# Optimization experiments

Hardware: AMD Instinct MI355X
Metric: run time of the kernel (lower is better)

## Reference

```python
import jax, jax.numpy as jnp
import numpy as np

N_NODES = 100000  # static segment count for segment_sum
DEGREE = 2        # polynomial degree of the Laplacian filter


def setup_inputs() -> dict:
    key = jax.random.key(0)
    k1, k2, k3, k4 = jax.random.split(key, 4)
    N, E, C = N_NODES, 1600000, 32
    x = jax.random.normal(k1, (N, C), dtype=jnp.float32)
    weights = jax.random.normal(k2, (1 + DEGREE,), dtype=jnp.float32)
    edge_src = jax.random.randint(k3, (E,), 0, N, dtype=jnp.int32)
    edge_dst = jax.random.randint(k4, (E,), 0, N, dtype=jnp.int32)
    return {"x": x, "weights": weights, "edge_src": edge_src, "edge_dst": edge_dst}


def reference(x, weights, edge_src, edge_dst):
    """y = (w0 * I + w1 * L + ... + w_d * L^d) @ x with L = D - A,
    computed by the recurrence t_k = L @ t_{k-1} (never materializing L^k)."""
    N = N_NODES
    # node degrees: D[i] = number of edges landing on i
    deg = jax.ops.segment_sum(jnp.ones_like(edge_src, dtype=x.dtype), edge_dst,
                              num_segments=N)  # [N]

    def lap_matvec(t):
        # (L @ t)[i] = deg[i] * t[i] - sum_{(s->i) in E} t[s]
        agg = jax.ops.segment_sum(t[edge_src], edge_dst, num_segments=N)  # [N, C]
        return deg[:, None] * t - agg

    y = weights[0] * x
    t = x
    for k in range(1, 1 + DEGREE):  # fixed small loop over polynomial order
        t = lap_matvec(t)
        y = y + weights[k] * t
    return y
```

## Files before the change

### kernel.cpp

```cpp
#include <hip/hip_runtime.h>

#define C 32
#define NT 256
#define BSH 8
#define BNODE 256
#define CAPC 5632
#define SRCMASK 0x1FFFF

typedef float f32x4 __attribute__((ext_vector_type(4)));

__device__ __forceinline__ unsigned int f2bf(float f) {
    unsigned int u = __float_as_uint(f);
    return (u + 0x7FFFu + ((u >> 16) & 1u)) >> 16;
}
__device__ __forceinline__ float bflo(unsigned int u) { return __uint_as_float(u << 16); }
__device__ __forceinline__ float bfhi(unsigned int u) { return __uint_as_float(u & 0xFFFF0000u); }

__global__ void init_cursor(int* __restrict__ cursor, int nbuck) {
    int i = blockIdx.x * blockDim.x + threadIdx.x;
    if (i < nbuck) cursor[i] = i * CAPC;
}

__global__ __launch_bounds__(1024) void phaseA(const int* __restrict__ src,
                                               const int* __restrict__ dst,
                                               int* __restrict__ cursor,
                                               int* __restrict__ pk,
                                               int E, int nbuck, int chunk) {
    extern __shared__ int l[];
    int* lcnt = l;
    int* lcur = l + nbuck;
    int tid = threadIdx.x;
    for (int i = tid; i < nbuck; i += 1024) lcnt[i] = 0;
    __syncthreads();
    int base = blockIdx.x * chunk;
    int end  = min(base + chunk, E);
    for (int e = base + tid; e < end; e += 1024)
        atomicAdd(&lcnt[dst[e] >> BSH], 1);
    __syncthreads();
    for (int i = tid; i < nbuck; i += 1024) {
        int c = lcnt[i];
        lcur[i] = c ? atomicAdd(&cursor[i], c) : 0;
    }
    __syncthreads();
    for (int e = base + tid; e < end; e += 1024) {
        int d = dst[e];
        int b = d >> BSH;
        int pos = atomicAdd(&lcur[b], 1);
        pk[pos] = src[e] | ((d & (BNODE - 1)) << 17);
    }
}

__global__ __launch_bounds__(512) void phaseB(int* __restrict__ pk,
                                              const int* __restrict__ cursor,
                                              int* __restrict__ row_start,
                                              int* __restrict__ ideg,
                                              const float* __restrict__ x,
                                              uint2* __restrict__ xb2, int N) {
    __shared__ int ent[CAPC];
    __shared__ int h[BNODE];
    __shared__ int s[BNODE];
    __shared__ int cur[BNODE];
    int b = blockIdx.x;
    int tid = threadIdx.x;

    int n0 = b << BSH;
    int nvalid = min(N - n0, BNODE);
    for (int i = tid; i < nvalid * 8; i += 512) {
        int n = n0 + (i >> 3);
        int lq = i & 7;
        const float* xp = x + (size_t)n * C + lq * 4;
        uint2 r;
        r.x = f2bf(xp[0]) | (f2bf(xp[1]) << 16);
        r.y = f2bf(xp[2]) | (f2bf(xp[3]) << 16);
        xb2[(size_t)n * 8 + lq] = r;
    }

    int base = b * CAPC;
    int cnt = min(cursor[b] - base, CAPC);
    for (int i = tid; i < cnt; i += 512) ent[i] = pk[base + i];
    if (tid < BNODE) h[tid] = 0;
    __syncthreads();
    for (int i = tid; i < cnt; i += 512) atomicAdd(&h[ent[i] >> 17], 1);
    __syncthreads();
    int v = 0;
    if (tid < BNODE) { v = h[tid]; s[tid] = v; }
    __syncthreads();
    for (int off = 1; off < BNODE; off <<= 1) {
        int u = 0;
        if (tid < BNODE && tid >= off) u = s[tid - off];
        __syncthreads();
        if (tid < BNODE) s[tid] += u;
        __syncthreads();
    }
    if (tid < BNODE) {
        int exc = s[tid] - v;
        int n = n0 + tid;
        if (n < N) { row_start[n] = base + exc; ideg[n] = v; }
        cur[tid] = exc;
    }
    __syncthreads();
    for (int i = tid; i < cnt; i += 512) {
        int en = ent[i];
        int pos = atomicAdd(&cur[en >> 17], 1);
        pk[base + pos] = en & SRCMASK;
    }
}

#define ACC4(u0, u1)                                     \
    a0 += bflo(u0); a1 += bfhi(u0);                      \
    a2 += bflo(u1); a3 += bfhi(u1);

__global__ __launch_bounds__(NT) void gather1_bf(const float* __restrict__ x,
        const uint2* __restrict__ xb2, const int* __restrict__ pk,
        const int* __restrict__ row_start, const int* __restrict__ ideg,
        float* __restrict__ t1, uint2* __restrict__ t1b2, int N) {
    int g = blockIdx.x * blockDim.x + threadIdx.x;
    int n = g >> 3;
    if (n >= N) return;
    int lq = g & 7;
    int rs = row_start[n];
    int dg = ideg[n];
    int re = rs + dg;
    float a0 = 0.f, a1 = 0.f, a2 = 0.f, a3 = 0.f;
    int j = rs;
    for (; j + 7 < re; j += 8) {
        int s0 = __builtin_nontemporal_load(&pk[j]);
        int s1 = __builtin_nontemporal_load(&pk[j + 1]);
        int s2 = __builtin_nontemporal_load(&pk[j + 2]);
        int s3 = __builtin_nontemporal_load(&pk[j + 3]);
        int s4 = __builtin_nontemporal_load(&pk[j + 4]);
        int s5 = __builtin_nontemporal_load(&pk[j + 5]);
        int s6 = __builtin_nontemporal_load(&pk[j + 6]);
        int s7 = __builtin_nontemporal_load(&pk[j + 7]);
        uint2 u0 = xb2[(size_t)s0 * 8 + lq];
        uint2 u1 = xb2[(size_t)s1 * 8 + lq];
        uint2 u2 = xb2[(size_t)s2 * 8 + lq];
        uint2 u3 = xb2[(size_t)s3 * 8 + lq];
        uint2 u4 = xb2[(size_t)s4 * 8 + lq];
        uint2 u5 = xb2[(size_t)s5 * 8 + lq];
        uint2 u6 = xb2[(size_t)s6 * 8 + lq];
        uint2 u7 = xb2[(size_t)s7 * 8 + lq];
        ACC4(u0.x, u0.y) ACC4(u1.x, u1.y) ACC4(u2.x, u2.y) ACC4(u3.x, u3.y)
        ACC4(u4.x, u4.y) ACC4(u5.x, u5.y) ACC4(u6.x, u6.y) ACC4(u7.x, u7.y)
    }
    for (; j + 1 < re; j += 2) {
        int s0 = __builtin_nontemporal_load(&pk[j]);
        int s1 = __builtin_nontemporal_load(&pk[j + 1]);
        uint2 u0 = xb2[(size_t)s0 * 8 + lq];
        uint2 u1 = xb2[(size_t)s1 * 8 + lq];
        ACC4(u0.x, u0.y) ACC4(u1.x, u1.y)
    }
    if (j < re) {
        uint2 u0 = xb2[(size_t)__builtin_nontemporal_load(&pk[j]) * 8 + lq];
        ACC4(u0.x, u0.y)
    }
    size_t o = (size_t)n * C + lq * 4;
    f32x4 xv = __builtin_nontemporal_load((const f32x4*)(x + o));
    float fdg = (float)dg;
    f32x4 tv;
    tv.x = fdg * xv.x - a0;
    tv.y = fdg * xv.y - a1;
    tv.z = fdg * xv.z - a2;
    tv.w = fdg * xv.w - a3;
    __builtin_nontemporal_store(tv, (f32x4*)(t1 + o));
    uint2 r;
    r.x = f2bf(tv.x) | (f2bf(tv.y) << 16);
    r.y = f2bf(tv.z) | (f2bf(tv.w) << 16);
    t1b2[(size_t)n * 8 + lq] = r;
}

__global__ __launch_bounds__(NT) void gather2_bf(const float* __restrict__ x,
        const float* __restrict__ t1, const uint2* __restrict__ t1b2,
        const int* __restrict__ pk, const int* __restrict__ row_start,
        const int* __restrict__ ideg, const float* __restrict__ wts,
        float* __restrict__ y, int N) {
    int g = blockIdx.x * blockDim.x + threadIdx.x;
    int n = g >> 3;
    if (n >= N) return;
    int lq = g & 7;
    int rs = row_start[n];
    int dg = ideg[n];
    int re = rs + dg;
    float a0 = 0.f, a1 = 0.f, a2 = 0.f, a3 = 0.f;
    int j = rs;
    for (; j + 7 < re; j += 8) {
        int s0 = __builtin_nontemporal_load(&pk[j]);
        int s1 = __builtin_nontemporal_load(&pk[j + 1]);
        int s2 = __builtin_nontemporal_load(&pk[j + 2]);
        int s3 = __builtin_nontemporal_load(&pk[j + 3]);
        int s4 = __builtin_nontemporal_load(&pk[j + 4]);
        int s5 = __builtin_nontemporal_load(&pk[j + 5]);
        int s6 = __builtin_nontemporal_load(&pk[j + 6]);
        int s7 = __builtin_nontemporal_load(&pk[j + 7]);
        uint2 u0 = t1b2[(size_t)s0 * 8 + lq];
        uint2 u1 = t1b2[(size_t)s1 * 8 + lq];
        uint2 u2 = t1b2[(size_t)s2 * 8 + lq];
        uint2 u3 = t1b2[(size_t)s3 * 8 + lq];
        uint2 u4 = t1b2[(size_t)s4 * 8 + lq];
        uint2 u5 = t1b2[(size_t)s5 * 8 + lq];
        uint2 u6 = t1b2[(size_t)s6 * 8 + lq];
        uint2 u7 = t1b2[(size_t)s7 * 8 + lq];
        ACC4(u0.x, u0.y) ACC4(u1.x, u1.y) ACC4(u2.x, u2.y) ACC4(u3.x, u3.y)
        ACC4(u4.x, u4.y) ACC4(u5.x, u5.y) ACC4(u6.x, u6.y) ACC4(u7.x, u7.y)
    }
    for (; j + 1 < re; j += 2) {
        int s0 = __builtin_nontemporal_load(&pk[j]);
        int s1 = __builtin_nontemporal_load(&pk[j + 1]);
        uint2 u0 = t1b2[(size_t)s0 * 8 + lq];
        uint2 u1 = t1b2[(size_t)s1 * 8 + lq];
        ACC4(u0.x, u0.y) ACC4(u1.x, u1.y)
    }
    if (j < re) {
        uint2 u0 = t1b2[(size_t)__builtin_nontemporal_load(&pk[j]) * 8 + lq];
        ACC4(u0.x, u0.y)
    }
    size_t o = (size_t)n * C + lq * 4;
    f32x4 xv = __builtin_nontemporal_load((const f32x4*)(x + o));
    f32x4 tv = __builtin_nontemporal_load((const f32x4*)(t1 + o));
    float w0 = wts[0], w1 = wts[1], w2 = wts[2];
    float fdg = (float)dg;
    f32x4 r;
    r.x = w0 * xv.x + w1 * tv.x + w2 * (fdg * tv.x - a0);
    r.y = w0 * xv.y + w1 * tv.y + w2 * (fdg * tv.y - a1);
    r.z = w0 * xv.z + w1 * tv.z + w2 * (fdg * tv.z - a2);
    r.w = w0 * xv.w + w1 * tv.w + w2 * (fdg * tv.w - a3);
    __builtin_nontemporal_store(r, (f32x4*)(y + o));
}

__global__ __launch_bounds__(NT) void gather1_f32(const float* __restrict__ x,
        const int* __restrict__ pk, const int* __restrict__ row_start,
        const int* __restrict__ ideg, float* __restrict__ t1, int N) {
    int g = blockIdx.x * blockDim.x + threadIdx.x;
    int n = g >> 5;
    if (n >= N) return;
    int ch = g & 31;
    int rs = row_start[n], dg = ideg[n], re = rs + dg;
    float a0 = 0, a1 = 0, a2 = 0, a3 = 0;
    int j = rs;
    for (; j + 3 < re; j += 4) {
        a0 += x[(size_t)pk[j] * C + ch];     a1 += x[(size_t)pk[j + 1] * C + ch];
        a2 += x[(size_t)pk[j + 2] * C + ch]; a3 += x[(size_t)pk[j + 3] * C + ch];
    }
    for (; j < re; ++j) a0 += x[(size_t)pk[j] * C + ch];
    size_t o = (size_t)n * C + ch;
    t1[o] = (float)dg * x[o] - ((a0 + a1) + (a2 + a3));
}
__global__ __launch_bounds__(NT) void gather2_f32(const float* __restrict__ x,
        const float* __restrict__ t1, const int* __restrict__ pk,
        const int* __restrict__ row_start, const int* __restrict__ ideg,
        const float* __restrict__ wts, float* __restrict__ y, int N) {
    int g = blockIdx.x * blockDim.x + threadIdx.x;
    int n = g >> 5;
    if (n >= N) return;
    int ch = g & 31;
    int rs = row_start[n], dg = ideg[n], re = rs + dg;
    float a0 = 0, a1 = 0, a2 = 0, a3 = 0;
    int j = rs;
    for (; j + 3 < re; j += 4) {
        a0 += t1[(size_t)pk[j] * C + ch];     a1 += t1[(size_t)pk[j + 1] * C + ch];
        a2 += t1[(size_t)pk[j + 2] * C + ch]; a3 += t1[(size_t)pk[j + 3] * C + ch];
    }
    for (; j < re; ++j) a0 += t1[(size_t)pk[j] * C + ch];
    size_t o = (size_t)n * C + ch;
    float tv = t1[o];
    y[o] = wts[0] * x[o] + wts[1] * tv + wts[2] * ((float)dg * tv - ((a0 + a1) + (a2 + a3)));
}

extern "C" void kernel_launch(void* const* d_in, const int* in_sizes, int n_in,
                              void* d_out, int out_size, void* d_ws, size_t ws_size,
                              hipStream_t stream) {
    const float* x    = (const float*)d_in[0];
    const float* wts  = (const float*)d_in[1];
    const int*   esrc = (const int*)d_in[2];
    const int*   edst = (const int*)d_in[3];
    float*       y    = (float*)d_out;

    const int N = in_sizes[0] / C;
    const int E = in_sizes[2];
    const int nbuck = (N + BNODE - 1) >> BSH;
    const int nc = N * C;

    char* p = (char*)d_ws;
    auto align16 = [](size_t s) { return (s + 15) & ~(size_t)15; };
    int* cursor    = (int*)p; p += align16((size_t)nbuck * 4);
    int* row_start = (int*)p; p += align16((size_t)N * 4);
    int* ideg      = (int*)p; p += align16((size_t)N * 4);
    int* pk        = (int*)p; p += align16((size_t)nbuck * CAPC * 4);
    float* t1      = (float*)p; p += align16((size_t)nc * 4);
    uint2* xb2     = (uint2*)p; p += align16((size_t)nc * 2);
    uint2* t1b2    = (uint2*)p; p += align16((size_t)nc * 2);
    bool bf_ok = (size_t)(p - (char*)d_ws) <= ws_size;

    init_cursor<<<(nbuck + NT - 1) / NT, NT, 0, stream>>>(cursor, nbuck);

    const int ABLK = 256;
    const int chunk = (E + ABLK - 1) / ABLK;
    const size_t lds_a = (size_t)nbuck * 2 * 4;
    phaseA<<<ABLK, 1024, lds_a, stream>>>(esrc, edst, cursor, pk, E, nbuck, chunk);
    phaseB<<<nbuck, 512, 0, stream>>>(pk, cursor, row_start, ideg, x, xb2, N);

    if (bf_ok) {
        const int gblocks = ((size_t)N * 8 + NT - 1) / NT;
        gather1_bf<<<gblocks, NT, 0, stream>>>(x, xb2, pk, row_start, ideg, t1, t1b2, N);
        gather2_bf<<<gblocks, NT, 0, stream>>>(x, t1, t1b2, pk, row_start, ideg, wts, y, N);
    } else {
        const int gblocks = ((size_t)N * 32 + NT - 1) / NT;
        gather1_f32<<<gblocks, NT, 0, stream>>>(x, pk, row_start, ideg, t1, N);
        gather2_f32<<<gblocks, NT, 0, stream>>>(x, t1, pk, row_start, ideg, wts, y, N);
    }
}
```

Measured before the change: 175.0 us.

## Split each gather into two passes by source-node half for cache locality

```diff
diff --git a/kernel.cpp b/kernel.cpp
--- a/kernel.cpp
+++ b/kernel.cpp
@@ -53,13 +53,15 @@
 __global__ __launch_bounds__(512) void phaseB(int* __restrict__ pk,
                                               const int* __restrict__ cursor,
                                               int* __restrict__ row_start,
+                                              int* __restrict__ idegA,
                                               int* __restrict__ ideg,
                                               const float* __restrict__ x,
-                                              uint2* __restrict__ xb2, int N) {
+                                              uint2* __restrict__ xb2,
+                                              int N, int NH) {
     __shared__ int ent[CAPC];
-    __shared__ int h[BNODE];
-    __shared__ int s[BNODE];
-    __shared__ int cur[BNODE];
+    __shared__ int h[512];
+    __shared__ int s[512];
+    __shared__ int cur[512];
     int b = blockIdx.x;
     int tid = threadIdx.x;
 
@@ -78,52 +80,50 @@
     int base = b * CAPC;
     int cnt = min(cursor[b] - base, CAPC);
     for (int i = tid; i < cnt; i += 512) ent[i] = pk[base + i];
-    if (tid < BNODE) h[tid] = 0;
-    __syncthreads();
-    for (int i = tid; i < cnt; i += 512) atomicAdd(&h[ent[i] >> 17], 1);
-    __syncthreads();
-    int v = 0;
-    if (tid < BNODE) { v = h[tid]; s[tid] = v; }
-    __syncthreads();
-    for (int off = 1; off < BNODE; off <<= 1) {
-        int u = 0;
-        if (tid < BNODE && tid >= off) u = s[tid - off];
-        __syncthreads();
-        if (tid < BNODE) s[tid] += u;
-        __syncthreads();
-    }
-    if (tid < BNODE) {
-        int exc = s[tid] - v;
-        int n = n0 + tid;
-        if (n < N) { row_start[n] = base + exc; ideg[n] = v; }
-        cur[tid] = exc;
-    }
+    h[tid] = 0;
     __syncthreads();
     for (int i = tid; i < cnt; i += 512) {
         int en = ent[i];
-        int pos = atomicAdd(&cur[en >> 17], 1);
+        int k = (((unsigned)en >> 17) << 1) | ((en & SRCMASK) >= NH ? 1 : 0);
+        atomicAdd(&h[k], 1);
+    }
+    __syncthreads();
+    int v = h[tid];
+    s[tid] = v;
+    __syncthreads();
+    for (int off = 1; off < 512; off <<= 1) {
+        int u = (tid >= off) ? s[tid - off] : 0;
+        __syncthreads();
+        s[tid] += u;
+        __syncthreads();
+    }
+    cur[tid] = s[tid] - v;
+    __syncthreads();
+    if (tid < BNODE) {
+        int n = n0 + tid;
+        if (n < N) {
+            int hA = h[2 * tid], hB = h[2 * tid + 1];
+            row_start[n] = base + (s[2 * tid] - hA);
+            idegA[n] = hA;
+            ideg[n]  = hA + hB;
+        }
+    }
+    __syncthreads();
+    for (int i = tid; i < cnt; i += 512) {
+        int en = ent[i];
+        int k = (((unsigned)en >> 17) << 1) | ((en & SRCMASK) >= NH ? 1 : 0);
+        int pos = atomicAdd(&cur[k], 1);
         pk[base + pos] = en & SRCMASK;
     }
 }
 
-#define ACC4(u0, u1)                                     \
-    a0 += bflo(u0); a1 += bfhi(u0);                      \
-    a2 += bflo(u1); a3 += bfhi(u1);
-
-__global__ __launch_bounds__(NT) void gather1_bf(const float* __restrict__ x,
-        const uint2* __restrict__ xb2, const int* __restrict__ pk,
-        const int* __restrict__ row_start, const int* __restrict__ ideg,
-        float* __restrict__ t1, uint2* __restrict__ t1b2, int N) {
-    int g = blockIdx.x * blockDim.x + threadIdx.x;
-    int n = g >> 3;
-    if (n >= N) return;
-    int lq = g & 7;
-    int rs = row_start[n];
-    int dg = ideg[n];
-    int re = rs + dg;
-    float a0 = 0.f, a1 = 0.f, a2 = 0.f, a3 = 0.f;
-    int j = rs;
-    for (; j + 7 < re; j += 8) {
+__device__ __forceinline__ void accum_seg(const uint2* __restrict__ arr,
+                                          const int* __restrict__ pk,
+                                          int lo, int hi, int lq,
+                                          float& a0, float& a1, float& a2, float& a3) {
+#define ACC4(ux, uy) { a0 += bflo(ux); a1 += bfhi(ux); a2 += bflo(uy); a3 += bfhi(uy); }
+    int j = lo;
+    for (; j + 7 < hi; j += 8) {
         int s0 = __builtin_nontemporal_load(&pk[j]);
         int s1 = __builtin_nontemporal_load(&pk[j + 1]);
         int s2 = __builtin_nontemporal_load(&pk[j + 2]);
@@ -132,36 +132,69 @@
         int s5 = __builtin_nontemporal_load(&pk[j + 5]);
         int s6 = __builtin_nontemporal_load(&pk[j + 6]);
         int s7 = __builtin_nontemporal_load(&pk[j + 7]);
-        uint2 u0 = xb2[(size_t)s0 * 8 + lq];
-        uint2 u1 = xb2[(size_t)s1 * 8 + lq];
-        uint2 u2 = xb2[(size_t)s2 * 8 + lq];
-        uint2 u3 = xb2[(size_t)s3 * 8 + lq];
-        uint2 u4 = xb2[(size_t)s4 * 8 + lq];
-        uint2 u5 = xb2[(size_t)s5 * 8 + lq];
-        uint2 u6 = xb2[(size_t)s6 * 8 + lq];
-        uint2 u7 = xb2[(size_t)s7 * 8 + lq];
+        uint2 u0 = arr[(size_t)s0 * 8 + lq];
+        uint2 u1 = arr[(size_t)s1 * 8 + lq];
+        uint2 u2 = arr[(size_t)s2 * 8 + lq];
+        uint2 u3 = arr[(size_t)s3 * 8 + lq];
+        uint2 u4 = arr[(size_t)s4 * 8 + lq];
+        uint2 u5 = arr[(size_t)s5 * 8 + lq];
+        uint2 u6 = arr[(size_t)s6 * 8 + lq];
+        uint2 u7 = arr[(size_t)s7 * 8 + lq];
         ACC4(u0.x, u0.y) ACC4(u1.x, u1.y) ACC4(u2.x, u2.y) ACC4(u3.x, u3.y)
         ACC4(u4.x, u4.y) ACC4(u5.x, u5.y) ACC4(u6.x, u6.y) ACC4(u7.x, u7.y)
     }
-    for (; j + 1 < re; j += 2) {
+    for (; j + 1 < hi; j += 2) {
         int s0 = __builtin_nontemporal_load(&pk[j]);
         int s1 = __builtin_nontemporal_load(&pk[j + 1]);
-        uint2 u0 = xb2[(size_t)s0 * 8 + lq];
-        uint2 u1 = xb2[(size_t)s1 * 8 + lq];
+        uint2 u0 = arr[(size_t)s0 * 8 + lq];
+        uint2 u1 = arr[(size_t)s1 * 8 + lq];
         ACC4(u0.x, u0.y) ACC4(u1.x, u1.y)
     }
-    if (j < re) {
-        uint2 u0 = xb2[(size_t)__builtin_nontemporal_load(&pk[j]) * 8 + lq];
+    if (j < hi) {
+        uint2 u0 = arr[(size_t)__builtin_nontemporal_load(&pk[j]) * 8 + lq];
         ACC4(u0.x, u0.y)
     }
+#undef ACC4
+}
+
+__global__ __launch_bounds__(NT) void g1A(const uint2* __restrict__ xb2,
+        const int* __restrict__ pk, const int* __restrict__ row_start,
+        const int* __restrict__ idegA, float* __restrict__ t1, int N) {
+    int g = blockIdx.x * blockDim.x + threadIdx.x;
+    int n = g >> 3;
+    if (n >= N) return;
+    int lq = g & 7;
+    int rs = row_start[n];
+    float a0 = 0.f, a1 = 0.f, a2 = 0.f, a3 = 0.f;
+    accum_seg(xb2, pk, rs, rs + idegA[n], lq, a0, a1, a2, a3);
+    size_t o = (size_t)n * C + lq * 4;
+    f32x4 p = { -a0, -a1, -a2, -a3 };
+    __builtin_nontemporal_store(p, (f32x4*)(t1 + o));
+}
+
+__global__ __launch_bounds__(NT) void g1B(const float* __restrict__ x,
+        const uint2* __restrict__ xb2, const int* __restrict__ pk,
+        const int* __restrict__ row_start, const int* __restrict__ idegA,
+        const int* __restrict__ ideg, float* __restrict__ t1,
+        uint2* __restrict__ t1b2, int N) {
+    int g = blockIdx.x * blockDim.x + threadIdx.x;
+    int n = g >> 3;
+    if (n >= N) return;
+    int lq = g & 7;
+    int rs = row_start[n];
+    int dA = idegA[n];
+    int dg = ideg[n];
+    float a0 = 0.f, a1 = 0.f, a2 = 0.f, a3 = 0.f;
+    accum_seg(xb2, pk, rs + dA, rs + dg, lq, a0, a1, a2, a3);
     size_t o = (size_t)n * C + lq * 4;
     f32x4 xv = __builtin_nontemporal_load((const f32x4*)(x + o));
+    f32x4 p  = __builtin_nontemporal_load((const f32x4*)(t1 + o));
     float fdg = (float)dg;
     f32x4 tv;
-    tv.x = fdg * xv.x - a0;
-    tv.y = fdg * xv.y - a1;
-    tv.z = fdg * xv.z - a2;
-    tv.w = fdg * xv.w - a3;
+    tv.x = fdg * xv.x + p.x - a0;
+    tv.y = fdg * xv.y + p.y - a1;
+    tv.z = fdg * xv.z + p.z - a2;
+    tv.w = fdg * xv.w + p.w - a3;
     __builtin_nontemporal_store(tv, (f32x4*)(t1 + o));
     uint2 r;
     r.x = f2bf(tv.x) | (f2bf(tv.y) << 16);
@@ -169,61 +202,47 @@
     t1b2[(size_t)n * 8 + lq] = r;
 }
 
-__global__ __launch_bounds__(NT) void gather2_bf(const float* __restrict__ x,
+__global__ __launch_bounds__(NT) void g2A(const uint2* __restrict__ t1b2,
+        const int* __restrict__ pk, const int* __restrict__ row_start,
+        const int* __restrict__ idegA, float* __restrict__ accb, int N) {
+    int g = blockIdx.x * blockDim.x + threadIdx.x;
+    int n = g >> 3;
+    if (n >= N) return;
+    int lq = g & 7;
+    int rs = row_start[n];
+    float a0 = 0.f, a1 = 0.f, a2 = 0.f, a3 = 0.f;
+    accum_seg(t1b2, pk, rs, rs + idegA[n], lq, a0, a1, a2, a3);
+    size_t o = (size_t)n * C + lq * 4;
+    f32x4 p = { -a0, -a1, -a2, -a3 };
+    __builtin_nontemporal_store(p, (f32x4*)(accb + o));
+}
+
+__global__ __launch_bounds__(NT) void g2B(const float* __restrict__ x,
         const float* __restrict__ t1, const uint2* __restrict__ t1b2,
         const int* __restrict__ pk, const int* __restrict__ row_start,
-        const int* __restrict__ ideg, const float* __restrict__ wts,
+        const int* __restrict__ idegA, const int* __restrict__ ideg,
+        const float* __restrict__ accb, const float* __restrict__ wts,
         float* __restrict__ y, int N) {
     int g = blockIdx.x * blockDim.x + threadIdx.x;
     int n = g >> 3;
     if (n >= N) return;
     int lq = g & 7;
     int rs = row_start[n];
+    int dA = idegA[n];
     int dg = ideg[n];
-    int re = rs + dg;
     float a0 = 0.f, a1 = 0.f, a2 = 0.f, a3 = 0.f;
-    int j = rs;
-    for (; j + 7 < re; j += 8) {
-        int s0 = __builtin_nontemporal_load(&pk[j]);
-        int s1 = __builtin_nontemporal_load(&pk[j + 1]);
-        int s2 = __builtin_nontemporal_load(&pk[j + 2]);
-        int s3 = __builtin_nontemporal_load(&pk[j + 3]);
-        int s4 = __builtin_nontemporal_load(&pk[j + 4]);
-        int s5 = __builtin_nontemporal_load(&pk[j + 5]);
-        int s6 = __builtin_nontemporal_load(&pk[j + 6]);
-        int s7 = __builtin_nontemporal_load(&pk[j + 7]);
-        uint2 u0 = t1b2[(size_t)s0 * 8 + lq];
-        uint2 u1 = t1b2[(size_t)s1 * 8 + lq];
-        uint2 u2 = t1b2[(size_t)s2 * 8 + lq];
-        uint2 u3 = t1b2[(size_t)s3 * 8 + lq];
-        uint2 u4 = t1b2[(size_t)s4 * 8 + lq];
-        uint2 u5 = t1b2[(size_t)s5 * 8 + lq];
-        uint2 u6 = t1b2[(size_t)s6 * 8 + lq];
-        uint2 u7 = t1b2[(size_t)s7 * 8 + lq];
-        ACC4(u0.x, u0.y) ACC4(u1.x, u1.y) ACC4(u2.x, u2.y) ACC4(u3.x, u3.y)
-        ACC4(u4.x, u4.y) ACC4(u5.x, u5.y) ACC4(u6.x, u6.y) ACC4(u7.x, u7.y)
-    }
-    for (; j + 1 < re; j += 2) {
-        int s0 = __builtin_nontemporal_load(&pk[j]);
-        int s1 = __builtin_nontemporal_load(&pk[j + 1]);
-        uint2 u0 = t1b2[(size_t)s0 * 8 + lq];
-        uint2 u1 = t1b2[(size_t)s1 * 8 + lq];
-        ACC4(u0.x, u0.y) ACC4(u1.x, u1.y)
-    }
-    if (j < re) {
-        uint2 u0 = t1b2[(size_t)__builtin_nontemporal_load(&pk[j]) * 8 + lq];
-        ACC4(u0.x, u0.y)
-    }
+    accum_seg(t1b2, pk, rs + dA, rs + dg, lq, a0, a1, a2, a3);
     size_t o = (size_t)n * C + lq * 4;
     f32x4 xv = __builtin_nontemporal_load((const f32x4*)(x + o));
     f32x4 tv = __builtin_nontemporal_load((const f32x4*)(t1 + o));
+    f32x4 p  = __builtin_nontemporal_load((const f32x4*)(accb + o));
     float w0 = wts[0], w1 = wts[1], w2 = wts[2];
     float fdg = (float)dg;
     f32x4 r;
-    r.x = w0 * xv.x + w1 * tv.x + w2 * (fdg * tv.x - a0);
-    r.y = w0 * xv.y + w1 * tv.y + w2 * (fdg * tv.y - a1);
-    r.z = w0 * xv.z + w1 * tv.z + w2 * (fdg * tv.z - a2);
-    r.w = w0 * xv.w + w1 * tv.w + w2 * (fdg * tv.w - a3);
+    r.x = w0 * xv.x + w1 * tv.x + w2 * (fdg * tv.x + p.x - a0);
+    r.y = w0 * xv.y + w1 * tv.y + w2 * (fdg * tv.y + p.y - a1);
+    r.z = w0 * xv.z + w1 * tv.z + w2 * (fdg * tv.z + p.z - a2);
+    r.w = w0 * xv.w + w1 * tv.w + w2 * (fdg * tv.w + p.w - a3);
     __builtin_nontemporal_store(r, (f32x4*)(y + o));
 }
 
@@ -277,6 +296,7 @@
 
     const int N = in_sizes[0] / C;
     const int E = in_sizes[2];
+    const int NH = N / 2;
     const int nbuck = (N + BNODE - 1) >> BSH;
     const int nc = N * C;
 
@@ -284,9 +304,11 @@
     auto align16 = [](size_t s) { return (s + 15) & ~(size_t)15; };
     int* cursor    = (int*)p; p += align16((size_t)nbuck * 4);
     int* row_start = (int*)p; p += align16((size_t)N * 4);
+    int* idegA     = (int*)p; p += align16((size_t)N * 4);
     int* ideg      = (int*)p; p += align16((size_t)N * 4);
     int* pk        = (int*)p; p += align16((size_t)nbuck * CAPC * 4);
     float* t1      = (float*)p; p += align16((size_t)nc * 4);
+    float* accb    = (float*)p; p += align16((size_t)nc * 4);
     uint2* xb2     = (uint2*)p; p += align16((size_t)nc * 2);
     uint2* t1b2    = (uint2*)p; p += align16((size_t)nc * 2);
     bool bf_ok = (size_t)(p - (char*)d_ws) <= ws_size;
@@ -297,12 +319,14 @@
     const int chunk = (E + ABLK - 1) / ABLK;
     const size_t lds_a = (size_t)nbuck * 2 * 4;
     phaseA<<<ABLK, 1024, lds_a, stream>>>(esrc, edst, cursor, pk, E, nbuck, chunk);
-    phaseB<<<nbuck, 512, 0, stream>>>(pk, cursor, row_start, ideg, x, xb2, N);
+    phaseB<<<nbuck, 512, 0, stream>>>(pk, cursor, row_start, idegA, ideg, x, xb2, N, NH);
 
     if (bf_ok) {
         const int gblocks = ((size_t)N * 8 + NT - 1) / NT;
-        gather1_bf<<<gblocks, NT, 0, stream>>>(x, xb2, pk, row_start, ideg, t1, t1b2, N);
-        gather2_bf<<<gblocks, NT, 0, stream>>>(x, t1, t1b2, pk, row_start, ideg, wts, y, N);
+        g1A<<<gblocks, NT, 0, stream>>>(xb2, pk, row_start, idegA, t1, N);
+        g1B<<<gblocks, NT, 0, stream>>>(x, xb2, pk, row_start, idegA, ideg, t1, t1b2, N);
+        g2A<<<gblocks, NT, 0, stream>>>(t1b2, pk, row_start, idegA, accb, N);
+        g2B<<<gblocks, NT, 0, stream>>>(x, t1, t1b2, pk, row_start, idegA, ideg, accb, wts, y, N);
     } else {
         const int gblocks = ((size_t)N * 32 + NT - 1) / NT;
         gather1_f32<<<gblocks, NT, 0, stream>>>(x, pk, row_start, ideg, t1, N);
```

Measured after the change: 197.1 us. 1.13x slower.

## Fuse all phases into one cooperative persistent kernel with grid syncs

Applied to the files above, without the earlier changes.

```diff
diff --git a/kernel.cpp b/kernel.cpp
--- a/kernel.cpp
+++ b/kernel.cpp
@@ -1,11 +1,16 @@
 #include <hip/hip_runtime.h>
+#include <hip/hip_cooperative_groups.h>
+
+namespace cg = cooperative_groups;
 
 #define C 32
+#define NTC 256
 #define NT 256
 #define BSH 8
 #define BNODE 256
 #define CAPC 5632
 #define SRCMASK 0x1FFFF
+#define MAXBUCK 400
 
 typedef float f32x4 __attribute__((ext_vector_type(4)));
 
@@ -15,6 +20,178 @@
 }
 __device__ __forceinline__ float bflo(unsigned int u) { return __uint_as_float(u << 16); }
 __device__ __forceinline__ float bfhi(unsigned int u) { return __uint_as_float(u & 0xFFFF0000u); }
+
+__device__ __forceinline__ void accum_seg(const uint2* __restrict__ arr,
+                                          const int* __restrict__ pk,
+                                          int lo, int hi, int lq,
+                                          float& a0, float& a1, float& a2, float& a3) {
+#define ACC4(ux, uy) { a0 += bflo(ux); a1 += bfhi(ux); a2 += bflo(uy); a3 += bfhi(uy); }
+    int j = lo;
+    for (; j + 7 < hi; j += 8) {
+        int s0 = __builtin_nontemporal_load(&pk[j]);
+        int s1 = __builtin_nontemporal_load(&pk[j + 1]);
+        int s2 = __builtin_nontemporal_load(&pk[j + 2]);
+        int s3 = __builtin_nontemporal_load(&pk[j + 3]);
+        int s4 = __builtin_nontemporal_load(&pk[j + 4]);
+        int s5 = __builtin_nontemporal_load(&pk[j + 5]);
+        int s6 = __builtin_nontemporal_load(&pk[j + 6]);
+        int s7 = __builtin_nontemporal_load(&pk[j + 7]);
+        uint2 u0 = arr[(size_t)s0 * 8 + lq];
+        uint2 u1 = arr[(size_t)s1 * 8 + lq];
+        uint2 u2 = arr[(size_t)s2 * 8 + lq];
+        uint2 u3 = arr[(size_t)s3 * 8 + lq];
+        uint2 u4 = arr[(size_t)s4 * 8 + lq];
+        uint2 u5 = arr[(size_t)s5 * 8 + lq];
+        uint2 u6 = arr[(size_t)s6 * 8 + lq];
+        uint2 u7 = arr[(size_t)s7 * 8 + lq];
+        ACC4(u0.x, u0.y) ACC4(u1.x, u1.y) ACC4(u2.x, u2.y) ACC4(u3.x, u3.y)
+        ACC4(u4.x, u4.y) ACC4(u5.x, u5.y) ACC4(u6.x, u6.y) ACC4(u7.x, u7.y)
+    }
+    for (; j + 1 < hi; j += 2) {
+        int s0 = __builtin_nontemporal_load(&pk[j]);
+        int s1 = __builtin_nontemporal_load(&pk[j + 1]);
+        uint2 u0 = arr[(size_t)s0 * 8 + lq];
+        uint2 u1 = arr[(size_t)s1 * 8 + lq];
+        ACC4(u0.x, u0.y) ACC4(u1.x, u1.y)
+    }
+    if (j < hi) {
+        uint2 u0 = arr[(size_t)__builtin_nontemporal_load(&pk[j]) * 8 + lq];
+        ACC4(u0.x, u0.y)
+    }
+#undef ACC4
+}
+
+__global__ __launch_bounds__(NTC) void gcn_coop(
+        const float* __restrict__ x, const int* __restrict__ esrc,
+        const int* __restrict__ edst, const float* __restrict__ wts,
+        float* __restrict__ y, int* __restrict__ cursor,
+        int* __restrict__ row_start, int* __restrict__ ideg,
+        int* __restrict__ pk, float* __restrict__ t1,
+        uint2* __restrict__ xb2, uint2* __restrict__ t1b2,
+        int N, int E, int nbuck, int chunk) {
+    cg::grid_group grid = cg::this_grid();
+    __shared__ int lcnt[MAXBUCK];
+    __shared__ int lcur[MAXBUCK];
+    __shared__ int ent[CAPC];
+    __shared__ int h[BNODE];
+    __shared__ int ss[BNODE];
+    __shared__ int cur[BNODE];
+    int tid = threadIdx.x;
+    int nb = gridDim.x;
+    int gthreads = nb * NTC;
+    int gid0 = blockIdx.x * NTC + tid;
+
+    for (int i = gid0; i < nbuck; i += gthreads) cursor[i] = 0;
+    grid.sync();
+
+    {
+        for (int i = tid; i < nbuck; i += NTC) lcnt[i] = 0;
+        __syncthreads();
+        int base = blockIdx.x * chunk;
+        int end  = min(base + chunk, E);
+        for (int e = base + tid; e < end; e += NTC)
+            atomicAdd(&lcnt[edst[e] >> BSH], 1);
+        __syncthreads();
+        for (int i = tid; i < nbuck; i += NTC) {
+            int c = lcnt[i];
+            lcur[i] = i * CAPC + (c ? atomicAdd(&cursor[i], c) : 0);
+        }
+        __syncthreads();
+        for (int e = base + tid; e < end; e += NTC) {
+            int d = edst[e];
+            int b = d >> BSH;
+            int pos = atomicAdd(&lcur[b], 1);
+            pk[pos] = esrc[e] | ((d & (BNODE - 1)) << 17);
+        }
+        int nc8 = N * 8;
+        for (int i = gid0; i < nc8; i += gthreads) {
+            const float* xp = x + (size_t)i * 4;
+            uint2 r;
+            r.x = f2bf(xp[0]) | (f2bf(xp[1]) << 16);
+            r.y = f2bf(xp[2]) | (f2bf(xp[3]) << 16);
+            xb2[i] = r;
+        }
+    }
+    grid.sync();
+
+    for (int b = blockIdx.x; b < nbuck; b += nb) {
+        int base = b * CAPC;
+        int cnt = min(cursor[b], CAPC);
+        for (int i = tid; i < cnt; i += NTC) ent[i] = pk[base + i];
+        if (tid < BNODE) h[tid] = 0;
+        __syncthreads();
+        for (int i = tid; i < cnt; i += NTC) atomicAdd(&h[ent[i] >> 17], 1);
+        __syncthreads();
+        int v = 0;
+        if (tid < BNODE) { v = h[tid]; ss[tid] = v; }
+        __syncthreads();
+        for (int off = 1; off < BNODE; off <<= 1) {
+            int u = 0;
+            if (tid < BNODE && tid >= off) u = ss[tid - off];
+            __syncthreads();
+            if (tid < BNODE) ss[tid] += u;
+            __syncthreads();
+        }
+        if (tid < BNODE) {
+            int exc = ss[tid] - v;
+            int n = (b << BSH) + tid;
+            if (n < N) { row_start[n] = base + exc; ideg[n] = v; }
+            cur[tid] = exc;
+        }
+        __syncthreads();
+        for (int i = tid; i < cnt; i += NTC) {
+            int en = ent[i];
+            int pos = atomicAdd(&cur[en >> 17], 1);
+            pk[base + pos] = en & SRCMASK;
+        }
+        __syncthreads();
+    }
+    grid.sync();
+
+    int total = N * 8;
+    for (int g = gid0; g < total; g += gthreads) {
+        int n = g >> 3;
+        int lq = g & 7;
+        int rs = row_start[n];
+        int dg = ideg[n];
+        float a0 = 0.f, a1 = 0.f, a2 = 0.f, a3 = 0.f;
+        accum_seg(xb2, pk, rs, rs + dg, lq, a0, a1, a2, a3);
+        size_t o = (size_t)n * C + lq * 4;
+        f32x4 xv = __builtin_nontemporal_load((const f32x4*)(x + o));
+        float fdg = (float)dg;
+        f32x4 tv;
+        tv.x = fdg * xv.x - a0;
+        tv.y = fdg * xv.y - a1;
+        tv.z = fdg * xv.z - a2;
+        tv.w = fdg * xv.w - a3;
+        __builtin_nontemporal_store(tv, (f32x4*)(t1 + o));
+        uint2 r;
+        r.x = f2bf(tv.x) | (f2bf(tv.y) << 16);
+        r.y = f2bf(tv.z) | (f2bf(tv.w) << 16);
+        t1b2[(size_t)n * 8 + lq] = r;
+    }
+    grid.sync();
+
+    float w0 = wts[0], w1 = wts[1], w2 = wts[2];
+    for (int g = gid0; g < total; g += gthreads) {
+        int n = g >> 3;
+        int lq = g & 7;
+        int rs = row_start[n];
+        int dg = ideg[n];
+        float a0 = 0.f, a1 = 0.f, a2 = 0.f, a3 = 0.f;
+        accum_seg(t1b2, pk, rs, rs + dg, lq, a0, a1, a2, a3);
+        size_t o = (size_t)n * C + lq * 4;
+        f32x4 xv = __builtin_nontemporal_load((const f32x4*)(x + o));
+        f32x4 tv = __builtin_nontemporal_load((const f32x4*)(t1 + o));
+        float fdg = (float)dg;
+        f32x4 r;
+        r.x = w0 * xv.x + w1 * tv.x + w2 * (fdg * tv.x - a0);
+        r.y = w0 * xv.y + w1 * tv.y + w2 * (fdg * tv.y - a1);
+        r.z = w0 * xv.z + w1 * tv.z + w2 * (fdg * tv.z - a2);
+        r.w = w0 * xv.w + w1 * tv.w + w2 * (fdg * tv.w - a3);
+        __builtin_nontemporal_store(r, (f32x4*)(y + o));
+    }
+}
 
 __global__ void init_cursor(int* __restrict__ cursor, int nbuck) {
     int i = blockIdx.x * blockDim.x + threadIdx.x;
@@ -62,7 +239,6 @@
     __shared__ int cur[BNODE];
     int b = blockIdx.x;
     int tid = threadIdx.x;
-
     int n0 = b << BSH;
     int nvalid = min(N - n0, BNODE);
     for (int i = tid; i < nvalid * 8; i += 512) {
@@ -74,7 +250,6 @@
         r.y = f2bf(xp[2]) | (f2bf(xp[3]) << 16);
         xb2[(size_t)n * 8 + lq] = r;
     }
-
     int base = b * CAPC;
     int cnt = min(cursor[b] - base, CAPC);
     for (int i = tid; i < cnt; i += 512) ent[i] = pk[base + i];
@@ -105,10 +280,6 @@
         pk[base + pos] = en & SRCMASK;
     }
 }
-
-#define ACC4(u0, u1)                                     \
-    a0 += bflo(u0); a1 += bfhi(u0);                      \
-    a2 += bflo(u1); a3 += bfhi(u1);
 
 __global__ __launch_bounds__(NT) void gather1_bf(const float* __restrict__ x,
         const uint2* __restrict__ xb2, const int* __restrict__ pk,
@@ -120,40 +291,8 @@
     int lq = g & 7;
     int rs = row_start[n];
     int dg = ideg[n];
-    int re = rs + dg;
     float a0 = 0.f, a1 = 0.f, a2 = 0.f, a3 = 0.f;
-    int j = rs;
-    for (; j + 7 < re; j += 8) {
-        int s0 = __builtin_nontemporal_load(&pk[j]);
-        int s1 = __builtin_nontemporal_load(&pk[j + 1]);
-        int s2 = __builtin_nontemporal_load(&pk[j + 2]);
-        int s3 = __builtin_nontemporal_load(&pk[j + 3]);
-        int s4 = __builtin_nontemporal_load(&pk[j + 4]);
-        int s5 = __builtin_nontemporal_load(&pk[j + 5]);
-        int s6 = __builtin_nontemporal_load(&pk[j + 6]);
-        int s7 = __builtin_nontemporal_load(&pk[j + 7]);
-        uint2 u0 = xb2[(size_t)s0 * 8 + lq];
-        uint2 u1 = xb2[(size_t)s1 * 8 + lq];
-        uint2 u2 = xb2[(size_t)s2 * 8 + lq];
-        uint2 u3 = xb2[(size_t)s3 * 8 + lq];
-        uint2 u4 = xb2[(size_t)s4 * 8 + lq];
-        uint2 u5 = xb2[(size_t)s5 * 8 + lq];
-        uint2 u6 = xb2[(size_t)s6 * 8 + lq];
-        uint2 u7 = xb2[(size_t)s7 * 8 + lq];
-        ACC4(u0.x, u0.y) ACC4(u1.x, u1.y) ACC4(u2.x, u2.y) ACC4(u3.x, u3.y)
-        ACC4(u4.x, u4.y) ACC4(u5.x, u5.y) ACC4(u6.x, u6.y) ACC4(u7.x, u7.y)
-    }
-    for (; j + 1 < re; j += 2) {
-        int s0 = __builtin_nontemporal_load(&pk[j]);
-        int s1 = __builtin_nontemporal_load(&pk[j + 1]);
-        uint2 u0 = xb2[(size_t)s0 * 8 + lq];
-        uint2 u1 = xb2[(size_t)s1 * 8 + lq];
-        ACC4(u0.x, u0.y) ACC4(u1.x, u1.y)
-    }
-    if (j < re) {
-        uint2 u0 = xb2[(size_t)__builtin_nontemporal_load(&pk[j]) * 8 + lq];
-        ACC4(u0.x, u0.y)
-    }
+    accum_seg(xb2, pk, rs, rs + dg, lq, a0, a1, a2, a3);
     size_t o = (size_t)n * C + lq * 4;
     f32x4 xv = __builtin_nontemporal_load((const f32x4*)(x + o));
     float fdg = (float)dg;
@@ -180,40 +319,8 @@
     int lq = g & 7;
     int rs = row_start[n];
     int dg = ideg[n];
-    int re = rs + dg;
     float a0 = 0.f, a1 = 0.f, a2 = 0.f, a3 = 0.f;
-    int j = rs;
-    for (; j + 7 < re; j += 8) {
-        int s0 = __builtin_nontemporal_load(&pk[j]);
-        int s1 = __builtin_nontemporal_load(&pk[j + 1]);
-        int s2 = __builtin_nontemporal_load(&pk[j + 2]);
-        int s3 = __builtin_nontemporal_load(&pk[j + 3]);
-        int s4 = __builtin_nontemporal_load(&pk[j + 4]);
-        int s5 = __builtin_nontemporal_load(&pk[j + 5]);
-        int s6 = __builtin_nontemporal_load(&pk[j + 6]);
-        int s7 = __builtin_nontemporal_load(&pk[j + 7]);
-        uint2 u0 = t1b2[(size_t)s0 * 8 + lq];
-        uint2 u1 = t1b2[(size_t)s1 * 8 + lq];
-        uint2 u2 = t1b2[(size_t)s2 * 8 + lq];
-        uint2 u3 = t1b2[(size_t)s3 * 8 + lq];
-        uint2 u4 = t1b2[(size_t)s4 * 8 + lq];
-        uint2 u5 = t1b2[(size_t)s5 * 8 + lq];
-        uint2 u6 = t1b2[(size_t)s6 * 8 + lq];
-        uint2 u7 = t1b2[(size_t)s7 * 8 + lq];
-        ACC4(u0.x, u0.y) ACC4(u1.x, u1.y) ACC4(u2.x, u2.y) ACC4(u3.x, u3.y)
-        ACC4(u4.x, u4.y) ACC4(u5.x, u5.y) ACC4(u6.x, u6.y) ACC4(u7.x, u7.y)
-    }
-    for (; j + 1 < re; j += 2) {
-        int s0 = __builtin_nontemporal_load(&pk[j]);
-        int s1 = __builtin_nontemporal_load(&pk[j + 1]);
-        uint2 u0 = t1b2[(size_t)s0 * 8 + lq];
-        uint2 u1 = t1b2[(size_t)s1 * 8 + lq];
-        ACC4(u0.x, u0.y) ACC4(u1.x, u1.y)
-    }
-    if (j < re) {
-        uint2 u0 = t1b2[(size_t)__builtin_nontemporal_load(&pk[j]) * 8 + lq];
-        ACC4(u0.x, u0.y)
-    }
+    accum_seg(t1b2, pk, rs, rs + dg, lq, a0, a1, a2, a3);
     size_t o = (size_t)n * C + lq * 4;
     f32x4 xv = __builtin_nontemporal_load((const f32x4*)(x + o));
     f32x4 tv = __builtin_nontemporal_load((const f32x4*)(t1 + o));
@@ -227,45 +334,6 @@
     __builtin_nontemporal_store(r, (f32x4*)(y + o));
 }
 
-__global__ __launch_bounds__(NT) void gather1_f32(const float* __restrict__ x,
-        const int* __restrict__ pk, const int* __restrict__ row_start,
-        const int* __restrict__ ideg, float* __restrict__ t1, int N) {
-    int g = blockIdx.x * blockDim.x + threadIdx.x;
-    int n = g >> 5;
-    if (n >= N) return;
-    int ch = g & 31;
-    int rs = row_start[n], dg = ideg[n], re = rs + dg;
-    float a0 = 0, a1 = 0, a2 = 0, a3 = 0;
-    int j = rs;
-    for (; j + 3 < re; j += 4) {
-        a0 += x[(size_t)pk[j] * C + ch];     a1 += x[(size_t)pk[j + 1] * C + ch];
-        a2 += x[(size_t)pk[j + 2] * C + ch]; a3 += x[(size_t)pk[j + 3] * C + ch];
-    }
-    for (; j < re; ++j) a0 += x[(size_t)pk[j] * C + ch];
-    size_t o = (size_t)n * C + ch;
-    t1[o] = (float)dg * x[o] - ((a0 + a1) + (a2 + a3));
-}
-__global__ __launch_bounds__(NT) void gather2_f32(const float* __restrict__ x,
-        const float* __restrict__ t1, const int* __restrict__ pk,
-        const int* __restrict__ row_start, const int* __restrict__ ideg,
-        const float* __restrict__ wts, float* __restrict__ y, int N) {
-    int g = blockIdx.x * blockDim.x + threadIdx.x;
-    int n = g >> 5;
-    if (n >= N) return;
-    int ch = g & 31;
-    int rs = row_start[n], dg = ideg[n], re = rs + dg;
-    float a0 = 0, a1 = 0, a2 = 0, a3 = 0;
-    int j = rs;
-    for (; j + 3 < re; j += 4) {
-        a0 += t1[(size_t)pk[j] * C + ch];     a1 += t1[(size_t)pk[j + 1] * C + ch];
-        a2 += t1[(size_t)pk[j + 2] * C + ch]; a3 += t1[(size_t)pk[j + 3] * C + ch];
-    }
-    for (; j < re; ++j) a0 += t1[(size_t)pk[j] * C + ch];
-    size_t o = (size_t)n * C + ch;
-    float tv = t1[o];
-    y[o] = wts[0] * x[o] + wts[1] * tv + wts[2] * ((float)dg * tv - ((a0 + a1) + (a2 + a3)));
-}
-
 extern "C" void kernel_launch(void* const* d_in, const int* in_sizes, int n_in,
                               void* d_out, int out_size, void* d_ws, size_t ws_size,
                               hipStream_t stream) {
@@ -277,7 +345,7 @@
 
     const int N = in_sizes[0] / C;
     const int E = in_sizes[2];
-    const int nbuck = (N + BNODE - 1) >> BSH;
+    int nbuck = (N + BNODE - 1) >> BSH;
     const int nc = N * C;
 
     char* p = (char*)d_ws;
@@ -289,23 +357,37 @@
     float* t1      = (float*)p; p += align16((size_t)nc * 4);
     uint2* xb2     = (uint2*)p; p += align16((size_t)nc * 2);
     uint2* t1b2    = (uint2*)p; p += align16((size_t)nc * 2);
-    bool bf_ok = (size_t)(p - (char*)d_ws) <= ws_size;
-
-    init_cursor<<<(nbuck + NT - 1) / NT, NT, 0, stream>>>(cursor, nbuck);
-
-    const int ABLK = 256;
-    const int chunk = (E + ABLK - 1) / ABLK;
-    const size_t lds_a = (size_t)nbuck * 2 * 4;
-    phaseA<<<ABLK, 1024, lds_a, stream>>>(esrc, edst, cursor, pk, E, nbuck, chunk);
-    phaseB<<<nbuck, 512, 0, stream>>>(pk, cursor, row_start, ideg, x, xb2, N);
-
-    if (bf_ok) {
+
+    int maxB = 0;
+    hipError_t qerr = hipOccupancyMaxActiveBlocksPerMultiprocessor(
+        &maxB, (const void*)gcn_coop, NTC, 0);
+    int NB = 0;
+    if (qerr == hipSuccess && maxB > 0) {
+        NB = maxB * 256;
+        if (NB > 1024) NB = 1024;
+    }
+    bool launched = false;
+    if (NB >= 256) {
+        int chunk = (E + NB - 1) / NB;
+        void* args[] = { (void*)&x, (void*)&esrc, (void*)&edst, (void*)&wts,
+                         (void*)&y, (void*)&cursor, (void*)&row_start,
+                         (void*)&ideg, (void*)&pk, (void*)&t1, (void*)&xb2,
+                         (void*)&t1b2, (void*)&N, (void*)&E, (void*)&nbuck,
+                         (void*)&chunk };
+        hipError_t lerr = hipLaunchCooperativeKernel(
+            (const void*)gcn_coop, dim3(NB), dim3(NTC), args, 0, stream);
+        launched = (lerr == hipSuccess);
+    }
+
+    if (!launched) {
+        init_cursor<<<(nbuck + NT - 1) / NT, NT, 0, stream>>>(cursor, nbuck);
+        const int ABLK = 256;
+        const int chunk = (E + ABLK - 1) / ABLK;
+        const size_t lds_a = (size_t)nbuck * 2 * 4;
+        phaseA<<<ABLK, 1024, lds_a, stream>>>(esrc, edst, cursor, pk, E, nbuck, chunk);
+        phaseB<<<nbuck, 512, 0, stream>>>(pk, cursor, row_start, ideg, x, xb2, N);
         const int gblocks = ((size_t)N * 8 + NT - 1) / NT;
         gather1_bf<<<gblocks, NT, 0, stream>>>(x, xb2, pk, row_start, ideg, t1, t1b2, N);
         gather2_bf<<<gblocks, NT, 0, stream>>>(x, t1, t1b2, pk, row_start, ideg, wts, y, N);
-    } else {
-        const int gblocks = ((size_t)N * 32 + NT - 1) / NT;
-        gather1_f32<<<gblocks, NT, 0, stream>>>(x, pk, row_start, ideg, t1, N);
-        gather2_f32<<<gblocks, NT, 0, stream>>>(x, t1, pk, row_start, ideg, wts, y, N);
-    }
-}
+    }
+}
```

Result: slower. 623.2 us (+256.0%).
